# Kernel optimization log

Hardware: AMD Instinct MI355X
Metric: run time of the kernel (lower is better)

Reference implementation:

```python
import jax, jax.numpy as jnp
import numpy as np

B, N, D = 4, 2048, 1024
H, DH = 16, 64
MAX_POS_EMB = 256
TOPK = 64


def setup_inputs() -> dict:
    key = jax.random.key(0)
    ks = jax.random.split(key, 8)
    s = 0.02
    inner = H * DH
    return {
        "x": jax.random.normal(ks[0], (B, N, D), jnp.float32),
        "gating_mask": jax.random.uniform(ks[1], (B, 1, N, 1), jnp.float32),
        "Wq": jax.random.normal(ks[2], (D, inner), jnp.float32) * s,
        "bq": jnp.zeros((inner,), jnp.float32),
        "Wkv": jax.random.normal(ks[3], (D, 2 * inner), jnp.float32) * s,
        "bkv": jnp.zeros((2 * inner,), jnp.float32),
        "Wo": jax.random.normal(ks[4], (inner, D), jnp.float32) * s,
        "bo": jnp.zeros((D,), jnp.float32),
        "rel_emb": jax.random.normal(ks[5], (MAX_POS_EMB, DH), jnp.float32) * s,
        "mask": jnp.ones((B, N), bool),
        "sparse_topk": TOPK,
    }


def reference(x, gating_mask, Wq, bq, Wkv, bkv, Wo, bo, rel_emb, mask, sparse_topk):
    b, n, d = x.shape
    h, dh = H, DH
    scale = dh ** -0.5
    mask_val = -jnp.finfo(x.dtype).max

    # projections -> [b, h, n, dh]
    q = (x @ Wq + bq).reshape(b, n, h, dh).transpose(0, 2, 1, 3)
    kv = x @ Wkv + bkv
    k = kv[..., : h * dh].reshape(b, n, h, dh).transpose(0, 2, 1, 3)
    v = kv[..., h * dh:].reshape(b, n, h, dh).transpose(0, 2, 1, 3)

    dots = jnp.einsum("bhid,bhjd->bhij", q, k) * scale  # [b,h,n,n]

    # relative positional bias: q . E[clip(i-j+M, 0, M-1)]
    seq = jnp.arange(n)
    dist = jnp.clip(seq[:, None] - seq[None, :] + MAX_POS_EMB, 0, MAX_POS_EMB - 1)
    qE = jnp.einsum("bhid,rd->bhir", q, rel_emb) * scale  # [b,h,n,R]
    pos_attn = jnp.take_along_axis(qE, dist[None, None, :, :], axis=-1)  # [b,h,n,n]
    dots = dots + pos_attn

    # padding mask: mask_i * mask_j
    full_mask = mask[:, None, :, None] & mask[:, None, None, :]
    dots = jnp.where(full_mask, dots, mask_val)

    # topk sparsification: keep only scores >= k-th largest per row
    top = jax.lax.top_k(dots, sparse_topk)[0]  # [b,h,n,topk]
    vk = top[..., -1:]
    dots = jnp.where(dots < vk, mask_val, dots)

    attn = jax.nn.softmax(dots, axis=-1)
    attn = attn * gating_mask

    out = jnp.einsum("bhij,bhjd->bhid", attn, v)
    out = out.transpose(0, 2, 1, 3).reshape(b, n, h * dh)
    return out @ Wo + bo
```

## Files before the change

### kernel.cpp

```cpp
#include <hip/hip_runtime.h>
#include <stdint.h>


typedef __attribute__((ext_vector_type(8))) short short8;
typedef __attribute__((ext_vector_type(4))) float floatx4;
typedef _Float16 f16x2 __attribute__((ext_vector_type(2)));

#define Bn   4
#define Nn   2048
#define Hn   16
#define BHn  (Bn*Hn)
#define DELTA 0.0025f

__device__ __forceinline__ float bf2f(unsigned short u) {
  union { unsigned int i; float f; } v; v.i = ((unsigned int)u) << 16; return v.f;
}
__device__ __forceinline__ unsigned short f2bf(float f) {
  union { float f; unsigned int i; } v; v.f = f;
  unsigned int r = v.i + 0x7fffu + ((v.i >> 16) & 1u);
  return (unsigned short)(r >> 16);
}
__device__ __forceinline__ floatx4 mfma16(short8 a, short8 b, floatx4 c) {
  return __builtin_amdgcn_mfma_f32_16x16x32_bf16(a, b, c, 0, 0, 0);
}
__device__ __forceinline__ void split2(float x, unsigned short& h, unsigned short& m) {
  h = f2bf(x);
  m = f2bf(x - bf2f(h));
}
__device__ __forceinline__ void split3(float x, unsigned short& h, unsigned short& m, unsigned short& l) {
  h = f2bf(x);
  float r = x - bf2f(h);
  m = f2bf(r);
  l = f2bf(r - bf2f(m));
}
__device__ __forceinline__ unsigned int mapf(float f) {
  union { _Float16 h; unsigned short s; } u; u.h = (_Float16)f;
  unsigned int b = (unsigned int)u.s;
  return (b & 0x8000u) ? (b ^ 0xFFFFu) : (b | 0x8000u);
}
__device__ __forceinline__ float unmapf(unsigned int c) {
  unsigned int b = (c & 0x8000u) ? (c ^ 0x8000u) : (c ^ 0xFFFFu);
  union { _Float16 h; unsigned short s; } u; u.s = (unsigned short)b;
  return (float)u.h;
}

__global__ __launch_bounds__(256)
void transpose_split3(const float* __restrict__ W,
                      unsigned short* __restrict__ T0,
                      unsigned short* __restrict__ T1,
                      unsigned short* __restrict__ T2,
                      int K, int Ncols)
{
  __shared__ float tile[32][33];
  int k0 = blockIdx.y * 32, n0 = blockIdx.x * 32;
  int tx = threadIdx.x & 31, ty = threadIdx.x >> 5;
  for (int s = 0; s < 32; s += 8)
    tile[ty + s][tx] = W[(size_t)(k0 + ty + s) * Ncols + n0 + tx];
  __syncthreads();
  for (int s = 0; s < 32; s += 8) {
    float x = tile[tx][ty + s];
    unsigned short h, m, l;
    split3(x, h, m, l);
    size_t o = (size_t)(n0 + ty + s) * K + k0 + tx;
    T0[o] = h; T1[o] = m; T2[o] = l;
  }
}

__global__ __launch_bounds__(256)
void transpose_split2(const float* __restrict__ W,
                      unsigned short* __restrict__ T0,
                      unsigned short* __restrict__ T1,
                      int K, int Ncols)
{
  __shared__ float tile[32][33];
  int k0 = blockIdx.y * 32, n0 = blockIdx.x * 32;
  int tx = threadIdx.x & 31, ty = threadIdx.x >> 5;
  for (int s = 0; s < 32; s += 8)
    tile[ty + s][tx] = W[(size_t)(k0 + ty + s) * Ncols + n0 + tx];
  __syncthreads();
  for (int s = 0; s < 32; s += 8) {
    float x = tile[tx][ty + s];
    unsigned short h, m;
    split2(x, h, m);
    size_t o = (size_t)(n0 + ty + s) * K + k0 + tx;
    T0[o] = h; T1[o] = m;
  }
}

__global__ __launch_bounds__(256)
void convert_bf16(const float* __restrict__ in, unsigned short* __restrict__ outp, int n) {
  int i = blockIdx.x * 256 + threadIdx.x;
  if (i < n) outp[i] = f2bf(in[i]);
}

__global__ __launch_bounds__(256)
void gemm_qkv(const float* __restrict__ A,
              const unsigned short* __restrict__ B0,
              const unsigned short* __restrict__ B1,
              const unsigned short* __restrict__ B2,
              const float* __restrict__ bias,
              float* __restrict__ O32,
              unsigned short* __restrict__ Oh,
              unsigned short* __restrict__ Om,
              _Float16* __restrict__ Vh,
              int K, float scale)
{
  __shared__ unsigned short lA[3][128 * 40];
  __shared__ unsigned short lB[3][128 * 40];
  const int tid = threadIdx.x;
  const int lane = tid & 63;
  const int m0 = blockIdx.y * 128, n0 = blockIdx.x * 128;
  const bool vblk = (n0 >= 1024);
  const int wid = tid >> 6, wm = wid >> 1, wn = wid & 1;
  const int fr = lane & 15, fq = lane >> 4;
  floatx4 acc[4][4] = {};

  for (int k0 = 0; k0 < K; k0 += 32) {
    __syncthreads();
    #pragma unroll
    for (int p = 0; p < 2; p++) {
      int c = tid + p * 256;
      int row = c >> 2, kc = (c & 3) * 8;
      size_t go = (size_t)(m0 + row) * K + k0 + kc;
      float4 v0 = *(const float4*)&A[go];
      float4 v1 = *(const float4*)&A[go + 4];
      union { unsigned short u[8]; uint4 q; } hh, mm, ll;
      float xs[8] = {v0.x, v0.y, v0.z, v0.w, v1.x, v1.y, v1.z, v1.w};
      #pragma unroll
      for (int e = 0; e < 8; e++) split3(xs[e], hh.u[e], mm.u[e], ll.u[e]);
      *(uint4*)&lA[0][row * 40 + kc] = hh.q;
      *(uint4*)&lA[1][row * 40 + kc] = mm.q;
      size_t bo = (size_t)(n0 + row) * K + k0 + kc;
      *(uint4*)&lB[0][row * 40 + kc] = *(const uint4*)&B0[bo];
      *(uint4*)&lB[1][row * 40 + kc] = *(const uint4*)&B1[bo];
      if (!vblk) {
        *(uint4*)&lA[2][row * 40 + kc] = ll.q;
        *(uint4*)&lB[2][row * 40 + kc] = *(const uint4*)&B2[bo];
      }
    }
    __syncthreads();
    short8 af0[4], af1[4], af2[4], bf0[4], bf1[4], bf2v[4];
    #pragma unroll
    for (int t = 0; t < 4; t++) {
      int ao = (wm * 64 + t * 16 + fr) * 40 + 8 * fq;
      int bo2 = (wn * 64 + t * 16 + fr) * 40 + 8 * fq;
      af0[t] = *(const short8*)&lA[0][ao];
      af1[t] = *(const short8*)&lA[1][ao];
      bf0[t] = *(const short8*)&lB[0][bo2];
      bf1[t] = *(const short8*)&lB[1][bo2];
      if (!vblk) {
        af2[t] = *(const short8*)&lA[2][ao];
        bf2v[t] = *(const short8*)&lB[2][bo2];
      }
    }
    #pragma unroll
    for (int mi = 0; mi < 4; mi++)
      #pragma unroll
      for (int ni = 0; ni < 4; ni++) {
        acc[mi][ni] = mfma16(af0[mi], bf0[ni], acc[mi][ni]);
        acc[mi][ni] = mfma16(af0[mi], bf1[ni], acc[mi][ni]);
        acc[mi][ni] = mfma16(af1[mi], bf0[ni], acc[mi][ni]);
        if (!vblk) {
          acc[mi][ni] = mfma16(af1[mi], bf1[ni], acc[mi][ni]);
          acc[mi][ni] = mfma16(af0[mi], bf2v[ni], acc[mi][ni]);
          acc[mi][ni] = mfma16(af2[mi], bf0[ni], acc[mi][ni]);
        }
      }
  }
  #pragma unroll
  for (int mi = 0; mi < 4; mi++)
    #pragma unroll
    for (int ni = 0; ni < 4; ni++) {
      int nl = n0 + wn * 64 + ni * 16 + fr;
      float bv = bias[nl];
      #pragma unroll
      for (int rg = 0; rg < 4; rg++) {
        int ml = m0 + wm * 64 + mi * 16 + fq * 4 + rg;
        float val = (acc[mi][ni][rg] + bv) * scale;
        int bb = ml >> 11, ii = ml & 2047;
        int hh2 = (nl & 1023) >> 6, dd = nl & 63;
        size_t idx = (((size_t)bb * Hn + hh2) * Nn + ii) * 64 + dd;
        if (!vblk) {
          O32[idx] = val;
          unsigned short h, m;
          split2(val, h, m);
          Oh[idx] = h; Om[idx] = m;
        } else {
          Vh[idx] = (_Float16)val;
        }
      }
    }
}

__global__ __launch_bounds__(256)
void gemm_out(const float* __restrict__ A,
              const unsigned short* __restrict__ B0,
              const unsigned short* __restrict__ B1,
              const float* __restrict__ bias,
              float* __restrict__ O32,
              int Ncols, int K)
{
  __shared__ unsigned short lA[2][128 * 40];
  __shared__ unsigned short lB[2][128 * 40];
  const int tid = threadIdx.x;
  const int lane = tid & 63;
  const int m0 = blockIdx.y * 128, n0 = blockIdx.x * 128;
  const int wid = tid >> 6, wm = wid >> 1, wn = wid & 1;
  const int fr = lane & 15, fq = lane >> 4;
  floatx4 acc[4][4] = {};

  for (int k0 = 0; k0 < K; k0 += 32) {
    __syncthreads();
    #pragma unroll
    for (int p = 0; p < 2; p++) {
      int c = tid + p * 256;
      int row = c >> 2, kc = (c & 3) * 8;
      size_t go = (size_t)(m0 + row) * K + k0 + kc;
      float4 v0 = *(const float4*)&A[go];
      float4 v1 = *(const float4*)&A[go + 4];
      union { unsigned short u[8]; uint4 q; } hh, mm;
      float xs[8] = {v0.x, v0.y, v0.z, v0.w, v1.x, v1.y, v1.z, v1.w};
      #pragma unroll
      for (int e = 0; e < 8; e++) split2(xs[e], hh.u[e], mm.u[e]);
      *(uint4*)&lA[0][row * 40 + kc] = hh.q;
      *(uint4*)&lA[1][row * 40 + kc] = mm.q;
      size_t bo = (size_t)(n0 + row) * K + k0 + kc;
      *(uint4*)&lB[0][row * 40 + kc] = *(const uint4*)&B0[bo];
      *(uint4*)&lB[1][row * 40 + kc] = *(const uint4*)&B1[bo];
    }
    __syncthreads();
    short8 af[2][4], bfr[2][4];
    #pragma unroll
    for (int s = 0; s < 2; s++)
      #pragma unroll
      for (int t = 0; t < 4; t++) {
        af[s][t]  = *(const short8*)&lA[s][(wm * 64 + t * 16 + fr) * 40 + 8 * fq];
        bfr[s][t] = *(const short8*)&lB[s][(wn * 64 + t * 16 + fr) * 40 + 8 * fq];
      }
    #pragma unroll
    for (int mi = 0; mi < 4; mi++)
      #pragma unroll
      for (int ni = 0; ni < 4; ni++) {
        acc[mi][ni] = mfma16(af[0][mi], bfr[0][ni], acc[mi][ni]);
        acc[mi][ni] = mfma16(af[0][mi], bfr[1][ni], acc[mi][ni]);
        acc[mi][ni] = mfma16(af[1][mi], bfr[0][ni], acc[mi][ni]);
      }
  }
  #pragma unroll
  for (int mi = 0; mi < 4; mi++)
    #pragma unroll
    for (int ni = 0; ni < 4; ni++) {
      int nl = n0 + wn * 64 + ni * 16 + fr;
      float bv = bias[nl];
      #pragma unroll
      for (int rg = 0; rg < 4; rg++) {
        int ml = m0 + wm * 64 + mi * 16 + fq * 4 + rg;
        O32[(size_t)ml * Ncols + nl] = acc[mi][ni][rg] + bv;
      }
    }
}

__global__ __launch_bounds__(1024, 8)
void attn_k(const unsigned short* __restrict__ qh,
            const unsigned short* __restrict__ qm,
            const unsigned short* __restrict__ kh,
            const unsigned short* __restrict__ km,
            const _Float16* __restrict__ vh,
            const float* __restrict__ q32,
            const float* __restrict__ k32,
            const unsigned short* __restrict__ relbf,
            const float* __restrict__ rel32,
            const float* __restrict__ gating,
            const int* __restrict__ topkp,
            float* __restrict__ inner)
{
  extern __shared__ char smem[];
  _Float16* S = (_Float16*)smem;
  unsigned short* Kt0 = (unsigned short*)(smem + 65536);
  unsigned short* Kt1 = Kt0 + 4096;
  _Float16* qE = (_Float16*)Kt0;

  const int wgid = blockIdx.x;
  const int xcd = wgid & 7;
  const int idx = wgid >> 3;
  const int bh = xcd * 8 + (idx >> 7);
  const int ib = idx & 127;
  const int i0 = ib * 16;
  const int b = bh >> 4, h = bh & 15;
  const int tid = threadIdx.x;
  const int lane = tid & 63, w = tid >> 6;
  const int fr = lane & 15, fq = lane >> 4;
  const int topk = topkp[0];
  const size_t kbase = (size_t)bh * Nn * 64;

  const size_t qoff = ((size_t)bh * Nn + i0) * 64;
  const size_t qf = qoff + (size_t)fr * 64 + 8 * fq;
  const short8 aqh0 = *(const short8*)&qh[qf];
  const short8 aqh1 = *(const short8*)&qh[qf + 32];
  const short8 aqm0 = *(const short8*)&qm[qf];
  const short8 aqm1 = *(const short8*)&qm[qf + 32];

  {
    const bool stager = (tid >= 512);
    const int sidx = tid & 511;
    const int srow = sidx >> 3, sch = sidx & 7;
    const int sdst = srow * 64 + ((sch ^ (srow & 7)) * 8);
    const size_t sgbase = kbase + (size_t)srow * 64 + sch * 8;
    uint4 rr = {};
    if (stager) {
      rr = *(const uint4*)&kh[sgbase];
      *(uint4*)&Kt0[sdst] = rr;
      rr = *(const uint4*)&kh[sgbase + 4096];
    }
    __syncthreads();

    for (int jt = 0; jt < 32; jt++) {
      if (stager) {
        unsigned short* Kn = (jt & 1) ? Kt0 : Kt1;
        if (jt + 1 < 32) *(uint4*)&Kn[sdst] = rr;
        if (jt + 2 < 32)
          rr = *(const uint4*)&kh[sgbase + (size_t)(jt + 2) * 4096];
      } else if ((jt & 1) == (w >> 2)) {
        const unsigned short* Kc = (jt & 1) ? Kt1 : Kt0;
        int wc = w & 3;
        int row16 = wc * 16 + fr, r7 = fr & 7;
        int b0 = row16 * 64 + ((fq ^ r7) * 8);
        int b1 = row16 * 64 + (((fq + 4) ^ r7) * 8);
        const size_t kf = kbase + (size_t)(jt * 64 + row16) * 64 + 8 * fq;
        __builtin_amdgcn_s_setprio(1);
        floatx4 c = {};
        short8 m0 = *(const short8*)&km[kf];
        short8 m1 = *(const short8*)&km[kf + 32];
        short8 h0 = *(const short8*)&Kc[b0];
        short8 h1 = *(const short8*)&Kc[b1];
        c = mfma16(aqh0, h0, c);
        c = mfma16(aqm0, h0, c);
        c = mfma16(aqh1, h1, c);
        c = mfma16(aqm1, h1, c);
        c = mfma16(aqh0, m0, c);
        c = mfma16(aqh1, m1, c);
        __builtin_amdgcn_s_setprio(0);
        int colsw = jt * 64 + ((wc ^ fq) * 16) + fr;
        #pragma unroll
        for (int rg = 0; rg < 4; rg++)
          S[(fq * 4 + rg) * 2048 + colsw] = (_Float16)c[rg];
      }
      __syncthreads();
    }
  }

  {
    size_t rf = (size_t)(w * 16 + fr) * 64 + 8 * fq;
    short8 rb0 = *(const short8*)&relbf[rf];
    short8 rb1 = *(const short8*)&relbf[rf + 32];
    floatx4 c = {};
    c = mfma16(aqh0, rb0, c); c = mfma16(aqh1, rb1, c);
    c = mfma16(aqm0, rb0, c); c = mfma16(aqm1, rb1, c);
    int colsw = ((w ^ fq) * 16) + fr;
    #pragma unroll
    for (int rg = 0; rg < 4; rg++)
      qE[(fq * 4 + rg) * 256 + colsw] = (_Float16)c[rg];
  }
  __syncthreads();

  const int r = w;
  const int i = i0 + r;
  const int X = (r >> 2) << 4;
  _Float16* S0 = S + r * 2048;
  const _Float16* qE0 = qE + r * 256;
  union pun { unsigned int u; f16x2 h; };
  pun cAp, cCp;
  cAp.h[0] = qE0[255 ^ X]; cAp.h[1] = cAp.h[0];
  cCp.h[0] = qE0[X];       cCp.h[1] = cCp.h[0];
  const int swl = (2 * lane) ^ X;

  unsigned int kk[16];
  unsigned int mh = 0, ml = 0;
  #pragma unroll
  for (int e = 0; e < 16; e++) {
    const int jb = 128 * e;
    pun sv, ev;
    sv.u = *(const unsigned int*)&S0[jb + swl];
    if (jb + 127 <= i) ev = cAp;
    else if (jb >= i + 256) ev = cCp;
    else {
      const int j0 = jb + 2 * lane;
      int c0 = i - j0 + 256; c0 = c0 < 0 ? 0 : (c0 > 255 ? 255 : c0);
      int c1 = i - j0 + 255; c1 = c1 < 0 ? 0 : (c1 > 255 ? 255 : c1);
      ev.h[0] = qE0[c0 ^ X]; ev.h[1] = qE0[c1 ^ X];
    }
    pun rv; rv.h = sv.h + ev.h;
    unsigned int u = rv.u;
    unsigned int sgn = (u >> 15) & 0x00010001u;
    unsigned int code = u ^ (sgn * 0x7FFFu + 0x80008000u);
    kk[e] = code;
    unsigned int chi = code & 0xFFFF0000u, clo = code << 16;
    mh = mh > chi ? mh : chi;
    ml = ml > clo ? ml : clo;
  }
  unsigned int umax = (mh > ml ? mh : ml) >> 16;
  unsigned int mxu = umax, mnu = umax;
  #pragma unroll
  for (int d = 1; d < 64; d <<= 1) {
    unsigned int o1 = (unsigned int)__shfl_xor((int)mxu, d);
    unsigned int o2 = (unsigned int)__shfl_xor((int)mnu, d);
    mxu = o1 > mxu ? o1 : mxu;
    mnu = o2 < mnu ? o2 : mnu;
  }
  const float mxv = unmapf(mxu);

  unsigned int lo = mnu, hi = mxu + 1;
  #pragma unroll 1
  for (int it = 0; it < 13; it++) {
    unsigned int mid = (lo + hi) >> 1;
    int cnt = 0;
    #pragma unroll
    for (int e = 0; e < 16; e++) {
      cnt += (int)__popcll(__ballot((kk[e] >> 16) >= mid));
      cnt += (int)__popcll(__ballot((kk[e] & 0xffffu) >= mid));
    }
    if (cnt >= topk) lo = mid; else hi = mid;
  }
  const float Cv = unmapf(hi) + 2.0f * DELTA;
  const float Lv = unmapf(lo) - 2.0f * DELTA;
  const unsigned int Cu = mapf(Cv) + 1;
  int Lsi = (int)mapf(Lv) - 1;
  const unsigned int Lu = Lsi < 0 ? 0u : (unsigned int)Lsi;

  char* sb = (char*)S0;
  unsigned int* Pk = (unsigned int*)sb;
  int*   Jc = (int*)(sb + 512);
  float* Sx = (float*)(sb + 768);
  float* P2 = (float*)(sb + 1024);
  asm volatile("" ::: "memory");
  const unsigned long long lmlt = (1ull << lane) - 1ull;

  int base = 0, mc = 0;
  #pragma unroll
  for (int t = 0; t < 32; t++) {
    unsigned int code = (t & 1) ? (kk[t >> 1] >> 16) : (kk[t >> 1] & 0xffffu);
    const int j = 2 * lane + 128 * (t >> 1) + (t & 1);
    bool dk = code >= Cu;
    bool cd = (code >= Lu) && !dk;
    unsigned long long mk = __ballot(dk);
    if (dk) { int pos = base + __popcll(mk & lmlt); Pk[pos] = (unsigned int)j | (code << 16); }
    base += __popcll(mk);
    mk = __ballot(cd);
    if (cd) { int pos = mc + __popcll(mk & lmlt); if (pos < 64) Jc[pos] = j; }
    mc += __popcll(mk);
  }
  if (mc > 64) mc = 64;
  asm volatile("" ::: "memory");

  const double qv = (double)q32[((size_t)bh * Nn + i) * 64 + lane];
  #pragma unroll 1
  for (int c2 = 0; c2 < mc; c2++) {
    int j = Jc[c2];
    int ridx = i - j + 256; ridx = ridx < 0 ? 0 : (ridx > 255 ? 255 : ridx);
    double t2 = qv * ((double)k32[((size_t)bh * Nn + j) * 64 + lane] +
                      (double)rel32[ridx * 64 + lane]);
    #pragma unroll
    for (int d = 1; d < 64; d <<= 1) t2 += __shfl_xor(t2, d);
    if (lane == 0) Sx[c2] = (float)t2;
  }
  asm volatile("" ::: "memory");

  const int need = topk - base;
  float myx = (lane < mc) ? Sx[lane] : -3.0e38f;
  int rank = 0;
  #pragma unroll 1
  for (int c2 = 0; c2 < mc; c2++) {
    float o = Sx[c2];
    rank += (o > myx || (o == myx && c2 < lane)) ? 1 : 0;
  }
  unsigned long long bm = __ballot((lane < mc) && (rank == need - 1));
  float vk = bm ? __shfl(myx, (int)__ffsll(bm) - 1) : 3.0e38f;
  bool ck = (lane < mc) && ((rank < need) || (myx == vk));
  unsigned long long km2 = __ballot(ck);
  float pb = 0.f;
  if (ck) {
    int pos = base + __popcll(km2 & lmlt);
    Pk[pos] = (unsigned int)Jc[lane];
    pb = __expf(myx - mxv);
    P2[pos] = pb;
  }
  const int nk = base + __popcll(km2);
  float ps = pb;
  #pragma unroll 1
  for (int t = lane; t < base; t += 64) {
    float val = unmapf(Pk[t] >> 16);
    float p = __expf(val - mxv);
    P2[t] = p; ps += p;
  }
  #pragma unroll
  for (int d = 1; d < 64; d <<= 1) ps += __shfl_xor(ps, d);
  const float coef = gating[(size_t)b * Nn + i] / ps;
  asm volatile("" ::: "memory");

  const _Float16* vbp = vh + (size_t)bh * Nn * 64 + lane;
  float a0 = 0.f, a1 = 0.f, a2 = 0.f, a3 = 0.f;
  #pragma unroll 1
  for (int t = 0; t < 64; t += 4) {
    int j0 = (int)(Pk[t] & 0xffffu), j1 = (int)(Pk[t + 1] & 0xffffu);
    int j2 = (int)(Pk[t + 2] & 0xffffu), j3 = (int)(Pk[t + 3] & 0xffffu);
    float p0 = P2[t], p1 = P2[t + 1], p2 = P2[t + 2], p3 = P2[t + 3];
    a0 += p0 * (float)vbp[(size_t)j0 * 64];
    a1 += p1 * (float)vbp[(size_t)j1 * 64];
    a2 += p2 * (float)vbp[(size_t)j2 * 64];
    a3 += p3 * (float)vbp[(size_t)j3 * 64];
  }
  #pragma unroll 1
  for (int t = 64; t < nk; t++)
    a0 += P2[t] * (float)vbp[(size_t)(Pk[t] & 0xffffu) * 64];
  inner[((size_t)b * Nn + i) * 1024 + h * 64 + lane] = (a0 + a1 + a2 + a3) * coef;
}

extern "C" void kernel_launch(void* const* d_in, const int* in_sizes, int n_in,
                              void* d_out, int out_size, void* d_ws, size_t ws_size,
                              hipStream_t stream) {
  const float* x      = (const float*)d_in[0];
  const float* gating = (const float*)d_in[1];
  const float* Wq     = (const float*)d_in[2];
  const float* bq     = (const float*)d_in[3];
  const float* Wkv    = (const float*)d_in[4];
  const float* bkv    = (const float*)d_in[5];
  const float* Wo     = (const float*)d_in[6];
  const float* bo     = (const float*)d_in[7];
  const float* rel    = (const float*)d_in[8];
  const int*   topk   = (const int*)d_in[10];
  float* out = (float*)d_out;

  char* ws = (char*)d_ws;
  size_t off = 0;
  auto alloc = [&](size_t bytes) -> void* {
    void* p = ws + off; off += (bytes + 255) & ~(size_t)255; return p;
  };
  unsigned short* Wqt0 = (unsigned short*)alloc(1024ull * 1024 * 2);
  unsigned short* Wqt1 = (unsigned short*)alloc(1024ull * 1024 * 2);
  unsigned short* Wqt2 = (unsigned short*)alloc(1024ull * 1024 * 2);
  unsigned short* Wkt0 = (unsigned short*)alloc(2048ull * 1024 * 2);
  unsigned short* Wkt1 = (unsigned short*)alloc(2048ull * 1024 * 2);
  unsigned short* Wkt2 = (unsigned short*)alloc(2048ull * 1024 * 2);
  unsigned short* Wot0 = (unsigned short*)alloc(1024ull * 1024 * 2);
  unsigned short* Wot1 = (unsigned short*)alloc(1024ull * 1024 * 2);
  unsigned short* relbf = (unsigned short*)alloc(256ull * 64 * 2);
  float* q32 = (float*)alloc((size_t)BHn * Nn * 64 * 4);
  float* k32 = (float*)alloc((size_t)BHn * Nn * 64 * 4);
  unsigned short* qhb = (unsigned short*)alloc((size_t)BHn * Nn * 64 * 2);
  unsigned short* qmb = (unsigned short*)alloc((size_t)BHn * Nn * 64 * 2);
  unsigned short* khb = (unsigned short*)alloc((size_t)BHn * Nn * 64 * 2);
  unsigned short* kmb = (unsigned short*)alloc((size_t)BHn * Nn * 64 * 2);
  _Float16* vhb = (_Float16*)alloc((size_t)BHn * Nn * 64 * 2);
  float* inner = (float*)alloc((size_t)Bn * Nn * 1024 * 4);
  if (off > ws_size) return;

  size_t shmem = 65536 + 16384;
  (void)hipFuncSetAttribute((const void*)attn_k,
                            hipFuncAttributeMaxDynamicSharedMemorySize, (int)shmem);

  transpose_split3<<<dim3(32, 32), 256, 0, stream>>>(Wq, Wqt0, Wqt1, Wqt2, 1024, 1024);
  transpose_split3<<<dim3(64, 32), 256, 0, stream>>>(Wkv, Wkt0, Wkt1, Wkt2, 1024, 2048);
  transpose_split2<<<dim3(32, 32), 256, 0, stream>>>(Wo, Wot0, Wot1, 1024, 1024);
  convert_bf16<<<dim3(64), 256, 0, stream>>>(rel, relbf, 256 * 64);

  gemm_qkv<<<dim3(8, 64), 256, 0, stream>>>(x, Wqt0, Wqt1, Wqt2, bq,
      q32, qhb, qmb, vhb, 1024, 0.125f);
  gemm_qkv<<<dim3(16, 64), 256, 0, stream>>>(x, Wkt0, Wkt1, Wkt2, bkv,
      k32, khb, kmb, vhb, 1024, 1.0f);

  attn_k<<<dim3(8192), 1024, shmem, stream>>>(qhb, qmb, khb, kmb, vhb,
      q32, k32, relbf, rel, gating, topk, inner);

  gemm_out<<<dim3(8, 64), 256, 0, stream>>>(inner, Wot0, Wot1, bo,
      out, 1024, 1024);
}
```

Baseline: 1.236 ms.

## Replace warp-specialized double-buffered K staging with single-buffer 128-row tiles

Drops the split where half the threads stage K tiles into a double buffer while the other half compute QK^T. All 1024 threads now cooperatively stage a 128-row K tile into one shared buffer, and 8 waves compute the scores, halving the number of outer iterations. This gives up producer/consumer overlap in exchange for fewer iterations and wider loads, at the cost of two barriers per iteration and idle waves during compute.

```diff
diff --git a/kernel.cpp b/kernel.cpp
--- a/kernel.cpp
+++ b/kernel.cpp
@@ -276,9 +276,8 @@
 {
   extern __shared__ char smem[];
   _Float16* S = (_Float16*)smem;
-  unsigned short* Kt0 = (unsigned short*)(smem + 65536);
-  unsigned short* Kt1 = Kt0 + 4096;
-  _Float16* qE = (_Float16*)Kt0;
+  unsigned short* Kt = (unsigned short*)(smem + 65536);
+  _Float16* qE = (_Float16*)Kt;
 
   const int wgid = blockIdx.x;
   const int xcd = wgid & 7;
@@ -301,53 +300,45 @@
   const short8 aqm1 = *(const short8*)&qm[qf + 32];
 
   {
-    const bool stager = (tid >= 512);
-    const int sidx = tid & 511;
-    const int srow = sidx >> 3, sch = sidx & 7;
+    const int srow = tid >> 3, sch = tid & 7;
     const int sdst = srow * 64 + ((sch ^ (srow & 7)) * 8);
     const size_t sgbase = kbase + (size_t)srow * 64 + sch * 8;
-    uint4 rr = {};
-    if (stager) {
-      rr = *(const uint4*)&kh[sgbase];
-      *(uint4*)&Kt0[sdst] = rr;
-      rr = *(const uint4*)&kh[sgbase + 4096];
-    }
-    __syncthreads();
-
-    for (int jt = 0; jt < 32; jt++) {
-      if (stager) {
-        unsigned short* Kn = (jt & 1) ? Kt0 : Kt1;
-        if (jt + 1 < 32) *(uint4*)&Kn[sdst] = rr;
-        if (jt + 2 < 32)
-          rr = *(const uint4*)&kh[sgbase + (size_t)(jt + 2) * 4096];
-      } else if ((jt & 1) == (w >> 2)) {
-        const unsigned short* Kc = (jt & 1) ? Kt1 : Kt0;
-        int wc = w & 3;
-        int row16 = wc * 16 + fr, r7 = fr & 7;
+    uint4 rr = *(const uint4*)&kh[sgbase];
+
+    for (int jt = 0; jt < 16; jt++) {
+      __syncthreads();
+      *(uint4*)&Kt[sdst] = rr;
+      if (jt + 1 < 16)
+        rr = *(const uint4*)&kh[sgbase + (size_t)(jt + 1) * 8192];
+      __syncthreads();
+      if (w < 8) {
+        int row16 = w * 16 + fr, r7 = fr & 7;
         int b0 = row16 * 64 + ((fq ^ r7) * 8);
         int b1 = row16 * 64 + (((fq + 4) ^ r7) * 8);
-        const size_t kf = kbase + (size_t)(jt * 64 + row16) * 64 + 8 * fq;
+        const size_t kf = kbase + (size_t)(jt * 128 + row16) * 64 + 8 * fq;
         __builtin_amdgcn_s_setprio(1);
         floatx4 c = {};
         short8 m0 = *(const short8*)&km[kf];
         short8 m1 = *(const short8*)&km[kf + 32];
-        short8 h0 = *(const short8*)&Kc[b0];
-        short8 h1 = *(const short8*)&Kc[b1];
-        c = mfma16(aqh0, h0, c);
-        c = mfma16(aqm0, h0, c);
-        c = mfma16(aqh1, h1, c);
-        c = mfma16(aqm1, h1, c);
+        {
+          short8 h0 = *(const short8*)&Kt[b0];
+          short8 h1 = *(const short8*)&Kt[b1];
+          c = mfma16(aqh0, h0, c);
+          c = mfma16(aqm0, h0, c);
+          c = mfma16(aqh1, h1, c);
+          c = mfma16(aqm1, h1, c);
+        }
         c = mfma16(aqh0, m0, c);
         c = mfma16(aqh1, m1, c);
         __builtin_amdgcn_s_setprio(0);
-        int colsw = jt * 64 + ((wc ^ fq) * 16) + fr;
+        int colsw = jt * 128 + ((w ^ fq) * 16) + fr;
         #pragma unroll
         for (int rg = 0; rg < 4; rg++)
           S[(fq * 4 + rg) * 2048 + colsw] = (_Float16)c[rg];
       }
-      __syncthreads();
-    }
-  }
+    }
+  }
+  __syncthreads();
 
   {
     size_t rf = (size_t)(w * 16 + fr) * 64 + 8 * fq;
```

New measurement: 1.188 ms. -3.9%, faster.
